# Optimization experiments

Measured on AMD Instinct MI355X. Metric: run time of the kernel, lower is better.

## Reference

```python
import jax, jax.numpy as jnp
import numpy as np


def setup_inputs() -> dict:
    key = jax.random.key(0)
    k1, k2, k3, k4 = jax.random.split(key, 4)
    C, R = 64, 8  # channels, reduced = channels // 8
    B, D, H, W = 2, 16, 16, 16
    x = jax.random.normal(k1, (B, C, D, H, W), dtype=jnp.float32)
    # 1x1x1 Conv3d kernels are plain [out_ch, in_ch] matrices (no bias)
    Wq = jax.random.normal(k2, (R, C), dtype=jnp.float32) * (C ** -0.5)
    Wk = jax.random.normal(k3, (R, C), dtype=jnp.float32) * (C ** -0.5)
    Wv = jax.random.normal(k4, (C, C), dtype=jnp.float32) * (C ** -0.5)
    gamma = jnp.ones((1,), dtype=jnp.float32) * 0.5  # nonzero so output depends on attention
    return {"x": x, "Wq": Wq, "Wk": Wk, "Wv": Wv, "gamma": gamma}


def reference(x, Wq, Wk, Wv, gamma):
    b, c, d, h, w = x.shape
    n = d * h * w
    xf = x.astype(jnp.float32).reshape(b, c, n)        # [b, c, n]
    q = jnp.einsum('rc,bcn->bnr', Wq, xf)              # [b, n, r]
    k = jnp.einsum('rc,bcn->brn', Wk, xf)              # [b, r, n]
    scale = q.shape[-1] ** -0.5
    attn = jax.nn.softmax(jnp.einsum('bnr,brm->bnm', q, k) * scale, axis=-1)  # [b, n_q, n_k]
    v = jnp.einsum('oc,bcn->bon', Wv, xf)              # [b, c, n]
    # out = value @ attn^T : out[b,c,q] = sum_k v[b,c,k] * attn[b,q,k]
    out = jnp.einsum('bck,bqk->bcq', v, attn).reshape(b, c, d, h, w)
    return x + gamma.astype(x.dtype) * out.astype(x.dtype)
```

## Files before the change

### kernel.cpp

```cpp
#include <hip/hip_runtime.h>
#include <math.h>

#define BB 2
#define CC 64
#define NN 4096
#define RR 8
#define KSPLIT 4
#define SCALE 0.35355339059327373f

typedef _Float16 f16x8 __attribute__((ext_vector_type(8)));
typedef _Float16 f16x4 __attribute__((ext_vector_type(4)));
typedef float f32x4 __attribute__((ext_vector_type(4)));

__global__ __launch_bounds__(256) void proj_kernel(
    const float* __restrict__ x, const float* __restrict__ Wq,
    const float* __restrict__ Wk, const float* __restrict__ Wv,
    _Float16* __restrict__ qh, _Float16* __restrict__ kh,
    _Float16* __restrict__ vph)
{
    const int t = (int)blockIdx.x * 256 + (int)threadIdx.x;
    const int grp = t >> 13;
    const int p = t & 8191;
    const int b = p >> 12;
    const int n = p & (NN - 1);
    const float* xp = x + (size_t)b * CC * NN + n;

    float xc[CC];
#pragma unroll
    for (int c = 0; c < CC; ++c) xc[c] = xp[(size_t)c * NN];

    const float* W = (grp == 0) ? Wq : (grp == 1) ? Wk
                                     : (Wv + (size_t)(grp - 2) * 8 * CC);
    float a[8];
#pragma unroll
    for (int j = 0; j < 8; ++j) a[j] = 0.f;
#pragma unroll
    for (int c = 0; c < CC; ++c) {
        const float xv = xc[c];
#pragma unroll
        for (int j = 0; j < 8; ++j)
            a[j] = fmaf(W[j * CC + c], xv, a[j]);
    }
    if (grp == 0) {
        f16x8 o;
#pragma unroll
        for (int j = 0; j < 8; ++j) o[j] = (_Float16)(a[j] * SCALE);
        *(f16x8*)(qh + ((size_t)b * NN + n) * 8) = o;
    } else if (grp == 1) {
        f16x8 o;
#pragma unroll
        for (int j = 0; j < 8; ++j) o[j] = (_Float16)a[j];
        *(f16x8*)(kh + ((size_t)b * NN + n) * 8) = o;
    } else {
        const int c0 = (grp - 2) * 8;
        _Float16* vb = vph + ((size_t)(b * 512 + (n >> 3)) * CC + c0) * 8 + (n & 7);
#pragma unroll
        for (int j = 0; j < 8; ++j) vb[j * 8] = (_Float16)a[j];
    }
}

__global__ __launch_bounds__(256) void attn_kernel(
    const _Float16* __restrict__ qh, const _Float16* __restrict__ kh,
    const _Float16* __restrict__ vph, _Float16* __restrict__ part_o,
    float* __restrict__ part_m, float* __restrict__ part_l)
{
    const int tid = (int)threadIdx.x;
    const int wid = tid >> 6;
    const int lane = tid & 63;
    const int lg = lane >> 4;
    const int lc = lane & 15;
    const int gw = (int)blockIdx.x * 4 + wid;
    const int qi = gw & 255;
    const int b  = (gw >> 8) & 1;
    const int ks = gw >> 9;
    const int q0 = qi * 16;

    const f16x8 zf = {};
    const f32x4 z4 = {};

    f16x8 qfrag = zf;
    if (lg == 0)
        qfrag = *(const f16x8*)(qh + ((size_t)b * NN + q0 + lc) * 8);

    float m = -1e30f, l = 0.f;
    f32x4 acc0 = z4, acc1 = z4, acc2 = z4, acc3 = z4;

    const _Float16* khb = kh + (size_t)b * NN * 8;
    const _Float16* vpb = vph + (size_t)b * 512 * CC * 8;

    for (int ch = 0; ch < 32; ++ch) {
        const int k0 = ks * 1024 + ch * 32;

        f16x8 kf0 = zf, kf1 = zf;
        if (lg == 0) {
            kf0 = *(const f16x8*)(khb + (size_t)(k0 + lc) * 8);
            kf1 = *(const f16x8*)(khb + (size_t)(k0 + 16 + lc) * 8);
        }
        f32x4 s0 = __builtin_amdgcn_mfma_f32_16x16x32_f16(kf0, qfrag, z4, 0, 0, 0);
        f32x4 s1 = __builtin_amdgcn_mfma_f32_16x16x32_f16(kf1, qfrag, z4, 0, 0, 0);

        float cm = fmaxf(fmaxf(fmaxf(s0[0], s0[1]), fmaxf(s0[2], s0[3])),
                         fmaxf(fmaxf(s1[0], s1[1]), fmaxf(s1[2], s1[3])));
        cm = fmaxf(cm, __shfl_xor(cm, 16));
        cm = fmaxf(cm, __shfl_xor(cm, 32));

        if (!__all(cm <= m)) {
            const float mnew = fmaxf(m, cm);
            const float alpha = __expf(m - mnew);
            m = mnew;
            l *= alpha;
            acc0 *= alpha; acc1 *= alpha; acc2 *= alpha; acc3 *= alpha;
        }

        float pr[8];
        float ls = 0.f;
#pragma unroll
        for (int v = 0; v < 4; ++v) { pr[v]     = __expf(s0[v] - m); ls += pr[v]; }
#pragma unroll
        for (int v = 0; v < 4; ++v) { pr[4 + v] = __expf(s1[v] - m); ls += pr[4 + v]; }
        ls += __shfl_xor(ls, 16);
        ls += __shfl_xor(ls, 32);
        l += ls;

        union { f16x4 h; unsigned u[2]; } P0, P1;
#pragma unroll
        for (int v = 0; v < 4; ++v) {
            P0.h[v] = (_Float16)pr[v];
            P1.h[v] = (_Float16)pr[4 + v];
        }
        const int sA = (((2 * lg) & 3) << 4) + lc;
        const int sB = (((2 * lg + 1) & 3) << 4) + lc;
        const unsigned t00 = __shfl(P0.u[0], sA), t01 = __shfl(P0.u[1], sA);
        const unsigned t10 = __shfl(P1.u[0], sA), t11 = __shfl(P1.u[1], sA);
        const unsigned u00 = __shfl(P0.u[0], sB), u01 = __shfl(P0.u[1], sB);
        const unsigned u10 = __shfl(P1.u[0], sB), u11 = __shfl(P1.u[1], sB);
        const bool hi = (lg & 2) != 0;
        union { unsigned u[4]; f16x8 v; } PF;
        PF.u[0] = hi ? t10 : t00;
        PF.u[1] = hi ? t11 : t01;
        PF.u[2] = hi ? u10 : u00;
        PF.u[3] = hi ? u11 : u01;

        const _Float16* vg = vpb + ((size_t)((k0 >> 3) + lg) * CC) * 8;
        f16x8 v0 = *(const f16x8*)(vg + (0 * 16 + lc) * 8);
        f16x8 v1 = *(const f16x8*)(vg + (1 * 16 + lc) * 8);
        f16x8 v2 = *(const f16x8*)(vg + (2 * 16 + lc) * 8);
        f16x8 v3 = *(const f16x8*)(vg + (3 * 16 + lc) * 8);
        acc0 = __builtin_amdgcn_mfma_f32_16x16x32_f16(v0, PF.v, acc0, 0, 0, 0);
        acc1 = __builtin_amdgcn_mfma_f32_16x16x32_f16(v1, PF.v, acc1, 0, 0, 0);
        acc2 = __builtin_amdgcn_mfma_f32_16x16x32_f16(v2, PF.v, acc2, 0, 0, 0);
        acc3 = __builtin_amdgcn_mfma_f32_16x16x32_f16(v3, PF.v, acc3, 0, 0, 0);
    }

    _Float16* po = part_o + (size_t)(ks * BB + b) * CC * NN + q0 + lc;
#pragma unroll
    for (int v = 0; v < 4; ++v) {
        po[(size_t)(0 * 16 + lg * 4 + v) * NN] = (_Float16)acc0[v];
        po[(size_t)(1 * 16 + lg * 4 + v) * NN] = (_Float16)acc1[v];
        po[(size_t)(2 * 16 + lg * 4 + v) * NN] = (_Float16)acc2[v];
        po[(size_t)(3 * 16 + lg * 4 + v) * NN] = (_Float16)acc3[v];
    }
    if (lane < 16) {
        part_m[(size_t)(ks * BB + b) * NN + q0 + lc] = m;
        part_l[(size_t)(ks * BB + b) * NN + q0 + lc] = l;
    }
}

__global__ __launch_bounds__(256) void merge_kernel(
    const float* __restrict__ x, const float* __restrict__ gamma,
    const _Float16* __restrict__ part_o, const float* __restrict__ part_m,
    const float* __restrict__ part_l, float* __restrict__ out)
{
    const int idx = (int)blockIdx.x * 256 + (int)threadIdx.x;
    const int n = idx & (NN - 1);
    const int b = idx >> 18;
    const float g = gamma[0];
    float mv[KSPLIT], lv[KSPLIT];
#pragma unroll
    for (int ks = 0; ks < KSPLIT; ++ks) {
        mv[ks] = part_m[(size_t)(ks * BB + b) * NN + n];
        lv[ks] = part_l[(size_t)(ks * BB + b) * NN + n];
    }
    float M = fmaxf(fmaxf(mv[0], mv[1]), fmaxf(mv[2], mv[3]));
    float L = 0.f, o = 0.f;
#pragma unroll
    for (int ks = 0; ks < KSPLIT; ++ks) {
        const float w = __expf(mv[ks] - M);
        L = fmaf(lv[ks], w, L);
        o = fmaf((float)part_o[(size_t)ks * (BB * CC * NN) + idx], w, o);
    }
    out[idx] = fmaf(g, o / L, x[idx]);
}

extern "C" void kernel_launch(void* const* d_in, const int* in_sizes, int n_in,
                              void* d_out, int out_size, void* d_ws, size_t ws_size,
                              hipStream_t stream)
{
    const float* x     = (const float*)d_in[0];
    const float* Wq    = (const float*)d_in[1];
    const float* Wk    = (const float*)d_in[2];
    const float* Wv    = (const float*)d_in[3];
    const float* gamma = (const float*)d_in[4];
    float* out = (float*)d_out;

    char* ws = (char*)d_ws;
    _Float16* qh     = (_Float16*)ws;
    _Float16* kh     = qh  + (size_t)BB * NN * 8;
    _Float16* vph    = kh  + (size_t)BB * NN * 8;
    _Float16* part_o = vph + (size_t)BB * 512 * CC * 8;
    float* part_m = (float*)(part_o + (size_t)KSPLIT * BB * CC * NN);
    float* part_l = part_m + (size_t)KSPLIT * BB * NN;

    hipLaunchKernelGGL(proj_kernel, dim3(320), dim3(256), 0, stream,
                       x, Wq, Wk, Wv, qh, kh, vph);
    hipLaunchKernelGGL(attn_kernel, dim3(512), dim3(256), 0, stream,
                       qh, kh, vph, part_o, part_m, part_l);
    hipLaunchKernelGGL(merge_kernel, dim3(BB * CC * NN / 256), dim3(256), 0, stream,
                       x, gamma, part_o, part_m, part_l, out);
}
```

Before: 106.2 us.

## Fuse split-K merge into attention kernel via in-block shared-memory reduction

Each block now owns a 16-query tile per batch, and its 8 waves each cover 512 keys, giving an 8-way in-block key split. Partial accumulators, max and sum go to shared memory and are merged inside the same kernel, which then writes the final residual output. This removes the separate merge kernel and the global round trip of the fp16 partial outputs and m/l arrays. The V loads are also moved ahead of the QK MFMA and the loop is unrolled to hide latency. In exchange, each block needs about 35KB of LDS and a block-wide barrier, and each wave's serial chain is shorter.

```diff
diff --git a/kernel.cpp b/kernel.cpp
--- a/kernel.cpp
+++ b/kernel.cpp
@@ -4,8 +4,6 @@
 #define BB 2
 #define CC 64
 #define NN 4096
-#define RR 8
-#define KSPLIT 4
 #define SCALE 0.35355339059327373f
 
 typedef _Float16 f16x8 __attribute__((ext_vector_type(8)));
@@ -59,21 +57,23 @@
     }
 }
 
-__global__ __launch_bounds__(256) void attn_kernel(
+__global__ __launch_bounds__(512) void attn_kernel(
     const _Float16* __restrict__ qh, const _Float16* __restrict__ kh,
-    const _Float16* __restrict__ vph, _Float16* __restrict__ part_o,
-    float* __restrict__ part_m, float* __restrict__ part_l)
+    const _Float16* __restrict__ vph, const float* __restrict__ x,
+    const float* __restrict__ gamma, float* __restrict__ out)
 {
     const int tid = (int)threadIdx.x;
     const int wid = tid >> 6;
     const int lane = tid & 63;
     const int lg = lane >> 4;
     const int lc = lane & 15;
-    const int gw = (int)blockIdx.x * 4 + wid;
-    const int qi = gw & 255;
-    const int b  = (gw >> 8) & 1;
-    const int ks = gw >> 9;
+    const int qi = (int)blockIdx.x & 255;
+    const int b  = (int)blockIdx.x >> 8;
     const int q0 = qi * 16;
+
+    __shared__ float sm_acc[8 * 64 * 17];
+    __shared__ float sm_m[8][16];
+    __shared__ float sm_l[8][16];
 
     const f16x8 zf = {};
     const f32x4 z4 = {};
@@ -87,15 +87,23 @@
 
     const _Float16* khb = kh + (size_t)b * NN * 8;
     const _Float16* vpb = vph + (size_t)b * 512 * CC * 8;
-
-    for (int ch = 0; ch < 32; ++ch) {
-        const int k0 = ks * 1024 + ch * 32;
+    const int kbase = wid * 512;
+
+#pragma unroll 4
+    for (int ch = 0; ch < 16; ++ch) {
+        const int k0 = kbase + ch * 32;
 
         f16x8 kf0 = zf, kf1 = zf;
         if (lg == 0) {
             kf0 = *(const f16x8*)(khb + (size_t)(k0 + lc) * 8);
             kf1 = *(const f16x8*)(khb + (size_t)(k0 + 16 + lc) * 8);
         }
+        const _Float16* vg = vpb + ((size_t)((k0 >> 3) + lg) * CC) * 8;
+        f16x8 v0 = *(const f16x8*)(vg + (0 * 16 + lc) * 8);
+        f16x8 v1 = *(const f16x8*)(vg + (1 * 16 + lc) * 8);
+        f16x8 v2 = *(const f16x8*)(vg + (2 * 16 + lc) * 8);
+        f16x8 v3 = *(const f16x8*)(vg + (3 * 16 + lc) * 8);
+
         f32x4 s0 = __builtin_amdgcn_mfma_f32_16x16x32_f16(kf0, qfrag, z4, 0, 0, 0);
         f32x4 s1 = __builtin_amdgcn_mfma_f32_16x16x32_f16(kf1, qfrag, z4, 0, 0, 0);
 
@@ -141,55 +149,46 @@
         PF.u[2] = hi ? u10 : u00;
         PF.u[3] = hi ? u11 : u01;
 
-        const _Float16* vg = vpb + ((size_t)((k0 >> 3) + lg) * CC) * 8;
-        f16x8 v0 = *(const f16x8*)(vg + (0 * 16 + lc) * 8);
-        f16x8 v1 = *(const f16x8*)(vg + (1 * 16 + lc) * 8);
-        f16x8 v2 = *(const f16x8*)(vg + (2 * 16 + lc) * 8);
-        f16x8 v3 = *(const f16x8*)(vg + (3 * 16 + lc) * 8);
         acc0 = __builtin_amdgcn_mfma_f32_16x16x32_f16(v0, PF.v, acc0, 0, 0, 0);
         acc1 = __builtin_amdgcn_mfma_f32_16x16x32_f16(v1, PF.v, acc1, 0, 0, 0);
         acc2 = __builtin_amdgcn_mfma_f32_16x16x32_f16(v2, PF.v, acc2, 0, 0, 0);
         acc3 = __builtin_amdgcn_mfma_f32_16x16x32_f16(v3, PF.v, acc3, 0, 0, 0);
     }
 
-    _Float16* po = part_o + (size_t)(ks * BB + b) * CC * NN + q0 + lc;
-#pragma unroll
-    for (int v = 0; v < 4; ++v) {
-        po[(size_t)(0 * 16 + lg * 4 + v) * NN] = (_Float16)acc0[v];
-        po[(size_t)(1 * 16 + lg * 4 + v) * NN] = (_Float16)acc1[v];
-        po[(size_t)(2 * 16 + lg * 4 + v) * NN] = (_Float16)acc2[v];
-        po[(size_t)(3 * 16 + lg * 4 + v) * NN] = (_Float16)acc3[v];
-    }
-    if (lane < 16) {
-        part_m[(size_t)(ks * BB + b) * NN + q0 + lc] = m;
-        part_l[(size_t)(ks * BB + b) * NN + q0 + lc] = l;
-    }
-}
-
-__global__ __launch_bounds__(256) void merge_kernel(
-    const float* __restrict__ x, const float* __restrict__ gamma,
-    const _Float16* __restrict__ part_o, const float* __restrict__ part_m,
-    const float* __restrict__ part_l, float* __restrict__ out)
-{
-    const int idx = (int)blockIdx.x * 256 + (int)threadIdx.x;
-    const int n = idx & (NN - 1);
-    const int b = idx >> 18;
-    const float g = gamma[0];
-    float mv[KSPLIT], lv[KSPLIT];
-#pragma unroll
-    for (int ks = 0; ks < KSPLIT; ++ks) {
-        mv[ks] = part_m[(size_t)(ks * BB + b) * NN + n];
-        lv[ks] = part_l[(size_t)(ks * BB + b) * NN + n];
-    }
-    float M = fmaxf(fmaxf(mv[0], mv[1]), fmaxf(mv[2], mv[3]));
-    float L = 0.f, o = 0.f;
-#pragma unroll
-    for (int ks = 0; ks < KSPLIT; ++ks) {
-        const float w = __expf(mv[ks] - M);
-        L = fmaf(lv[ks], w, L);
-        o = fmaf((float)part_o[(size_t)ks * (BB * CC * NN) + idx], w, o);
-    }
-    out[idx] = fmaf(g, o / L, x[idx]);
+    if (lane < 16) { sm_m[wid][lc] = m; sm_l[wid][lc] = l; }
+    {
+        float* sa = sm_acc + (size_t)wid * 64 * 17 + lc;
+#pragma unroll
+        for (int v = 0; v < 4; ++v) {
+            sa[(0 * 16 + lg * 4 + v) * 17] = acc0[v];
+            sa[(1 * 16 + lg * 4 + v) * 17] = acc1[v];
+            sa[(2 * 16 + lg * 4 + v) * 17] = acc2[v];
+            sa[(3 * 16 + lg * 4 + v) * 17] = acc3[v];
+        }
+    }
+    __syncthreads();
+
+    {
+        const int c = tid >> 3;
+        const int qb2 = (tid & 7) * 2;
+        const float g = gamma[0];
+#pragma unroll
+        for (int dq = 0; dq < 2; ++dq) {
+            const int q = qb2 + dq;
+            float M = sm_m[0][q];
+#pragma unroll
+            for (int w = 1; w < 8; ++w) M = fmaxf(M, sm_m[w][q]);
+            float L = 0.f, O = 0.f;
+#pragma unroll
+            for (int w = 0; w < 8; ++w) {
+                const float e = __expf(sm_m[w][q] - M);
+                L = fmaf(sm_l[w][q], e, L);
+                O = fmaf(sm_acc[(w * 64 + c) * 17 + q], e, O);
+            }
+            const size_t oi = (size_t)b * CC * NN + (size_t)c * NN + q0 + q;
+            out[oi] = fmaf(g, O / L, x[oi]);
+        }
+    }
 }
 
 extern "C" void kernel_launch(void* const* d_in, const int* in_sizes, int n_in,
@@ -204,17 +203,12 @@
     float* out = (float*)d_out;
 
     char* ws = (char*)d_ws;
-    _Float16* qh     = (_Float16*)ws;
-    _Float16* kh     = qh  + (size_t)BB * NN * 8;
-    _Float16* vph    = kh  + (size_t)BB * NN * 8;
-    _Float16* part_o = vph + (size_t)BB * 512 * CC * 8;
-    float* part_m = (float*)(part_o + (size_t)KSPLIT * BB * CC * NN);
-    float* part_l = part_m + (size_t)KSPLIT * BB * NN;
+    _Float16* qh  = (_Float16*)ws;
+    _Float16* kh  = qh + (size_t)BB * NN * 8;
+    _Float16* vph = kh + (size_t)BB * NN * 8;
 
     hipLaunchKernelGGL(proj_kernel, dim3(320), dim3(256), 0, stream,
                        x, Wq, Wk, Wv, qh, kh, vph);
-    hipLaunchKernelGGL(attn_kernel, dim3(512), dim3(256), 0, stream,
-                       qh, kh, vph, part_o, part_m, part_l);
-    hipLaunchKernelGGL(merge_kernel, dim3(BB * CC * NN / 256), dim3(256), 0, stream,
-                       x, gamma, part_o, part_m, part_l, out);
+    hipLaunchKernelGGL(attn_kernel, dim3(BB * 256), dim3(512), 0, stream,
+                       qh, kh, vph, x, gamma, out);
 }
```

After: 90.53 us. -14.8%, faster.
